# Kernel tuning notes

Hardware: AMD Instinct MI355X
Metric: run time of the kernel (lower is better)

Reference implementation:

```python
import jax, jax.numpy as jnp
import numpy as np
import math

N_HEAD = 32
ROPE_BASE = 10000.0


def _rope_headwise(x):
    # Faithful to the source bug: x is [B, H, S, D] and the rotary module uses
    # x.shape[1] (= H) as the "sequence length", so the angle depends on the
    # head index, broadcast over the true sequence axis.
    B, H, S, D = x.shape
    inv_freq = 1.0 / (ROPE_BASE ** (jnp.arange(0, D, 2, dtype=jnp.float32) / D))  # [D/2]
    t = jnp.arange(H, dtype=jnp.float32)                                          # [H]
    freqs = t[:, None] * inv_freq[None, :]                                        # [H, D/2]
    # emb = cat(freqs, freqs)[..., :D//2] == freqs, so cos/sin are just over freqs
    cos = jnp.cos(freqs)[None, :, None, :]   # [1, H, 1, D/2]
    sin = jnp.sin(freqs)[None, :, None, :]
    x1, x2 = x[..., : D // 2], x[..., D // 2 :]
    return jnp.concatenate([x1 * cos - x2 * sin, x1 * sin + x2 * cos], axis=-1)


def setup_inputs() -> dict:
    key = jax.random.key(0)
    ks = jax.random.split(key, 5)
    B, S, E = 2, 2048, 2048
    scale = 0.02
    return {
        "x": jax.random.normal(ks[0], (B, S, E), dtype=jnp.float32),
        "Wq": jax.random.normal(ks[1], (E, E), dtype=jnp.float32) * scale,
        "bq": jnp.zeros((E,), dtype=jnp.float32),
        "Wk": jax.random.normal(ks[2], (E, E), dtype=jnp.float32) * scale,
        "bk": jnp.zeros((E,), dtype=jnp.float32),
        "Wv": jax.random.normal(ks[3], (E, E), dtype=jnp.float32) * scale,
        "bv": jnp.zeros((E,), dtype=jnp.float32),
        "Wo": jax.random.normal(ks[4], (E, E), dtype=jnp.float32) * scale,
        "bo": jnp.zeros((E,), dtype=jnp.float32),
    }


def reference(x, Wq, bq, Wk, bk, Wv, bv, Wo, bo):
    B, S, E = x.shape
    H = N_HEAD
    D = E // H

    def split_heads(y):  # [B,S,E] -> [B,H,S,D]
        return y.reshape(B, S, H, D).transpose(0, 2, 1, 3)

    q = split_heads(x @ Wq + bq)
    k = split_heads(x @ Wk + bk)
    v = split_heads(x @ Wv + bv)

    q = _rope_headwise(q)
    k = _rope_headwise(k)

    scores = jnp.einsum("bhqd,bhkd->bhqk", q, k) / math.sqrt(D)  # [B,H,S,S]
    causal = jnp.triu(jnp.ones((S, S), dtype=bool), k=1)
    scores = jnp.where(causal[None, None], -jnp.inf, scores)
    attn = jax.nn.softmax(scores, axis=-1)
    out = jnp.einsum("bhqk,bhkd->bhqd", attn, v)                 # [B,H,S,D]
    out = out.transpose(0, 2, 1, 3).reshape(B, S, E)
    return out @ Wo + bo
```

## Files before the change

### kernel.cpp

```cpp
#include <hip/hip_runtime.h>
#include <hip/hip_bf16.h>

#define B_ 2
#define S_ 2048
#define E_ 2048
#define H_ 32
#define M_ (B_*S_)

typedef __bf16 bf16x8 __attribute__((ext_vector_type(8)));
typedef float  f32x4  __attribute__((ext_vector_type(4)));

__device__ __forceinline__ ushort f2bf(float f) {
    uint u = __float_as_uint(f);
    u += 0x7fffu + ((u >> 16) & 1u);
    return (ushort)(u >> 16);
}
__device__ __forceinline__ uint pack2bf(float a, float b) {
    __hip_bfloat162 h = __float22bfloat162_rn(make_float2(a, b));
    return *(uint*)&h;
}
__device__ __forceinline__ float fexp2(float x) {
#if __has_builtin(__builtin_amdgcn_exp2f)
    return __builtin_amdgcn_exp2f(x);
#else
    return exp2f(x);
#endif
}
__device__ __forceinline__ f32x4 f4zero() {
    f32x4 z; z[0]=0.f; z[1]=0.f; z[2]=0.f; z[3]=0.f; return z;
}
__device__ __forceinline__ void async16(const ushort* g, ushort* l) {
    __builtin_amdgcn_global_load_lds((const __attribute__((address_space(1))) void*)g,
                                     (__attribute__((address_space(3))) void*)l, 16, 0, 0);
}

#define NCAST ((M_*E_)/1024)
__global__ __launch_bounds__(256) void prep_kernel(const float* __restrict__ x, ushort* __restrict__ xb,
        const float* __restrict__ W0, const float* __restrict__ W1,
        const float* __restrict__ W2, const float* __restrict__ W3,
        ushort* __restrict__ T0, ushort* __restrict__ T1,
        ushort* __restrict__ T2, ushort* __restrict__ T3) {
    const int bid = blockIdx.x;
    if (bid < NCAST) {
        int i = (bid * 256 + threadIdx.x) * 4;
        float4 v = *(const float4*)(x + i);
        uint2 o;
        o.x = pack2bf(v.x, v.y);
        o.y = pack2bf(v.z, v.w);
        *(uint2*)(xb + i) = o;
        return;
    }
    const int wb = bid - NCAST;
    const int z  = wb >> 10;
    const int rem = wb & 1023;
    const float* W = (z==0)?W0:(z==1)?W1:(z==2)?W2:W3;
    ushort*      T = (z==0)?T0:(z==1)?T1:(z==2)?T2:T3;
    __shared__ float tile[64][65];
    const int k0 = (rem >> 5) * 64, n0 = (rem & 31) * 64;
    const int rr = threadIdx.x >> 4;
    const int cc = (threadIdx.x & 15) * 4;
    #pragma unroll
    for (int p = 0; p < 4; ++p) {
        int r = p * 16 + rr;
        float4 v = *(const float4*)(W + (size_t)(k0 + r) * E_ + n0 + cc);
        tile[r][cc+0] = v.x; tile[r][cc+1] = v.y; tile[r][cc+2] = v.z; tile[r][cc+3] = v.w;
    }
    __syncthreads();
    #pragma unroll
    for (int p = 0; p < 4; ++p) {
        int rn = p * 16 + rr;
        uint2 o;
        o.x = pack2bf(tile[cc+0][rn], tile[cc+1][rn]);
        o.y = pack2bf(tile[cc+2][rn], tile[cc+3][rn]);
        *(uint2*)(T + (size_t)(n0 + rn) * E_ + k0 + cc) = o;
    }
}

#define VMW4 asm volatile("s_waitcnt vmcnt(4)" ::: "memory")
#define VMW0 asm volatile("s_waitcnt vmcnt(0)" ::: "memory")
#define MEMB asm volatile("" ::: "memory")

#define STA_(bf, kt, h) { _Pragma("unroll") for (int it_ = 0; it_ < 2; ++it_) { \
    async16(A + (size_t)(m0 + it_*128 + (h)*64 + srow) * E_ + (kt)*64 + scg*8,  \
            &As[bf][(it_*128 + (h)*64 + wave*8) * 64]); } }

#define STB_(bf, kt, h) { _Pragma("unroll") for (int it_ = 0; it_ < 2; ++it_) { \
    int rih_ = it_*64 + srow;                                                   \
    int ldr_ = ((rih_ >> 5) << 6) + (h)*32 + (rih_ & 31);                       \
    int rwb_ = it_*64 + wave*8;                                                 \
    int wbs_ = ((rwb_ >> 5) << 6) + (h)*32 + (rwb_ & 31);                       \
    async16(Bt + (size_t)(n0 + ldr_) * E_ + (kt)*64 + scg*8,                    \
            &Bs[bf][wbs_ * 64]); } }

#define PH4_(bf, mh, LB, STAGES) {                                              \
    _Pragma("unroll") for (int m_ = 0; m_ < 4; ++m_)                            \
      _Pragma("unroll") for (int k_ = 0; k_ < 2; ++k_) {                        \
        int row_ = wm*128 + (mh)*64 + m_*16 + l15;                              \
        pa[m_][k_] = *(const bf16x8*)(&As[bf][row_*64 + (((k_*4 + quad) ^ (row_ & 7)) << 3)]); } \
    if (LB) {                                                                   \
      _Pragma("unroll") for (int n_ = 0; n_ < 4; ++n_)                          \
        _Pragma("unroll") for (int k_ = 0; k_ < 2; ++k_) {                      \
          int row_ = wn*64 + n_*16 + l15;                                       \
          pb[n_][k_] = *(const bf16x8*)(&Bs[bf][row_*64 + (((k_*4 + quad) ^ (row_ & 7)) << 3)]); } } \
    STAGES;                                                                     \
    MEMB; __builtin_amdgcn_s_barrier();                                         \
    __builtin_amdgcn_s_setprio(1);                                              \
    _Pragma("unroll") for (int k_ = 0; k_ < 2; ++k_)                            \
      _Pragma("unroll") for (int m_ = 0; m_ < 4; ++m_)                          \
        _Pragma("unroll") for (int n_ = 0; n_ < 4; ++n_)                        \
          acc[(mh)*4+m_][n_] = __builtin_amdgcn_mfma_f32_16x16x32_bf16(         \
              pa[m_][k_], pb[n_][k_], acc[(mh)*4+m_][n_], 0, 0, 0);             \
    __builtin_amdgcn_s_setprio(0);                                              \
    asm volatile("s_waitcnt lgkmcnt(0)" ::: "memory");                          \
    __builtin_amdgcn_sched_barrier(0);                                          \
    MEMB; __builtin_amdgcn_s_barrier(); MEMB;                                   \
  }

template<bool OUTF32, bool DOROPE, int NZ>
__global__ __launch_bounds__(512, 2) void gemm256(const ushort* __restrict__ A,
        const ushort* __restrict__ Bt0, const ushort* __restrict__ Bt1, const ushort* __restrict__ Bt2,
        const float* __restrict__ bias0, const float* __restrict__ bias1, const float* __restrict__ bias2,
        void* __restrict__ C0, void* __restrict__ C1, void* __restrict__ C2) {
    const int bid = blockIdx.x;
    const int z   = bid % NZ;
    const int nb  = (bid / NZ) % (E_ / 256);
    const int mb  = bid / (NZ * (E_ / 256));

    const ushort* Bt  = (z==0)?Bt0:(z==1)?Bt1:Bt2;
    const float* bias = (z==0)?bias0:(z==1)?bias1:bias2;
    void* Cv          = (z==0)?C0:(z==1)?C1:C2;

    __shared__ ushort As[2][256 * 64];
    __shared__ ushort Bs[2][256 * 64];

    const int tid  = threadIdx.x;
    const int wave = tid >> 6, lane = tid & 63;
    const int quad = lane >> 4, l15 = lane & 15;
    const int wm = wave >> 2, wn = wave & 3;
    const int m0 = mb * 256, n0 = nb * 256;
    const int srow = tid >> 3;
    const int scg  = (tid & 7) ^ (srow & 7);

    f32x4 acc[8][4];
    #pragma unroll
    for (int i = 0; i < 8; ++i)
        #pragma unroll
        for (int j = 0; j < 4; ++j) acc[i][j] = f4zero();

    bf16x8 pa[4][2];
    bf16x8 pb[4][2];

    STA_(0, 0, 0); STB_(0, 0, 0); STA_(0, 0, 1); STB_(0, 0, 1);
    STA_(1, 1, 0); STB_(1, 1, 0);
    VMW4;
    MEMB; __builtin_amdgcn_s_barrier(); MEMB;

    #pragma unroll 1
    for (int i = 0; i < 15; ++i) {
        const int t1 = 2*i + 1, t2 = 2*i + 2, t3 = 2*i + 3;
        PH4_(0, 0, 1, STB_(1, t1, 1); STA_(1, t1, 1));
        PH4_(0, 1, 0, STA_(0, t2, 0); STB_(0, t2, 0); VMW4);
        PH4_(1, 0, 1, STB_(0, t2, 1); STA_(0, t2, 1));
        PH4_(1, 1, 0, STA_(1, t3, 0); STB_(1, t3, 0); VMW4);
    }
    PH4_(0, 0, 1, STB_(1, 31, 1); STA_(1, 31, 1));
    PH4_(0, 1, 0, VMW0);
    PH4_(1, 0, 1, {});
    PH4_(1, 1, 0, {});

    if (DOROPE && z != 2) {
        const float qsc = (z == 0) ? 0.125f * 1.44269504f : 1.0f;
        const int h = (n0 + wn * 64) >> 6;
        float sn[2], cs[2];
        #pragma unroll
        for (int nt = 0; nt < 2; ++nt) {
            int j = nt * 16 + l15;
            float ang = (float)h * __expf(-(float)j * 0.28782313662425575f);
            __sincosf(ang, &sn[nt], &cs[nt]);
        }
        ushort* C = (ushort*)Cv;
        #pragma unroll
        for (int f = 0; f < 8; ++f) {
            #pragma unroll
            for (int nt = 0; nt < 2; ++nt) {
                int col1 = n0 + wn * 64 + nt * 16 + l15;
                float b1 = bias[col1], b2 = bias[col1 + 32];
                #pragma unroll
                for (int r = 0; r < 4; ++r) {
                    int rowg = m0 + wm * 128 + f * 16 + quad * 4 + r;
                    float x1 = acc[f][nt][r] + b1;
                    float x2 = acc[f][nt + 2][r] + b2;
                    C[(size_t)rowg * E_ + col1]      = f2bf((x1 * cs[nt] - x2 * sn[nt]) * qsc);
                    C[(size_t)rowg * E_ + col1 + 32] = f2bf((x1 * sn[nt] + x2 * cs[nt]) * qsc);
                }
            }
        }
    } else {
        #pragma unroll
        for (int f = 0; f < 8; ++f) {
            #pragma unroll
            for (int nt = 0; nt < 4; ++nt) {
                int col = n0 + wn * 64 + nt * 16 + l15;
                float bv = bias[col];
                #pragma unroll
                for (int r = 0; r < 4; ++r) {
                    int rowg = m0 + wm * 128 + f * 16 + quad * 4 + r;
                    float v = acc[f][nt][r] + bv;
                    if (OUTF32) ((float*)Cv)[(size_t)rowg * E_ + col] = v;
                    else        ((ushort*)Cv)[(size_t)rowg * E_ + col] = f2bf(v);
                }
            }
        }
    }
}
#undef STA_
#undef STB_
#undef PH4_

template<bool OUTF32, bool DOROPE, bool DOVT, int NZ>
__global__ __launch_bounds__(256) void gemm128(const ushort* __restrict__ A,
        const ushort* __restrict__ Bt0, const ushort* __restrict__ Bt1, const ushort* __restrict__ Bt2,
        const float* __restrict__ bias0, const float* __restrict__ bias1, const float* __restrict__ bias2,
        void* __restrict__ C0, void* __restrict__ C1, void* __restrict__ C2) {
    const int bid = blockIdx.x;
    const int z   = bid % NZ;
    const int nb  = (bid / NZ) % (E_ / 128);
    const int mb  = bid / (NZ * (E_ / 128));

    const ushort* Bt  = (z==0)?Bt0:(z==1)?Bt1:Bt2;
    const float* bias = (z==0)?bias0:(z==1)?bias1:bias2;
    void* Cv          = (z==0)?C0:(z==1)?C1:C2;

    __shared__ ushort smem[2 * 128 * 64];
    ushort* As = smem;
    ushort* Bs = smem + 128 * 64;

    const int tid  = threadIdx.x;
    const int wave = tid >> 6, lane = tid & 63;
    const int quad = lane >> 4, l15 = lane & 15;
    const int wm = wave >> 1, wn = wave & 1;
    const int m0 = mb * 128, n0 = nb * 128;
    const int srow = tid >> 3;
    const int scgx = (tid & 7) ^ (srow & 7);

    f32x4 acc[4][4];
    #pragma unroll
    for (int i = 0; i < 4; ++i)
        #pragma unroll
        for (int j = 0; j < 4; ++j) acc[i][j] = f4zero();

    for (int k0 = 0; k0 < E_; k0 += 64) {
        #pragma unroll
        for (int it = 0; it < 4; ++it) {
            int r = it * 32 + srow;
            async16(A  + (size_t)(m0 + r) * E_ + k0 + scgx * 8, As + (it * 256 + wave * 64) * 8);
            async16(Bt + (size_t)(n0 + r) * E_ + k0 + scgx * 8, Bs + (it * 256 + wave * 64) * 8);
        }
        __syncthreads();
        #pragma unroll
        for (int kk = 0; kk < 2; ++kk) {
            bf16x8 af[4], bfr[4];
            #pragma unroll
            for (int mt = 0; mt < 4; ++mt) {
                int row = wm * 64 + mt * 16 + l15;
                af[mt] = *(const bf16x8*)(As + row * 64 + (((kk * 4 + quad) ^ (row & 7)) << 3));
            }
            #pragma unroll
            for (int nt = 0; nt < 4; ++nt) {
                int row = wn * 64 + nt * 16 + l15;
                bfr[nt] = *(const bf16x8*)(Bs + row * 64 + (((kk * 4 + quad) ^ (row & 7)) << 3));
            }
            #pragma unroll
            for (int mt = 0; mt < 4; ++mt)
                #pragma unroll
                for (int nt = 0; nt < 4; ++nt)
                    acc[mt][nt] = __builtin_amdgcn_mfma_f32_16x16x32_bf16(af[mt], bfr[nt], acc[mt][nt], 0, 0, 0);
        }
        __syncthreads();
    }

    if (DOVT) {
        ushort* tbuf = smem;
        ushort* VT = (ushort*)Cv;
        const int b  = m0 >> 11;
        const int s0 = m0 & (S_ - 1);
        #pragma unroll 1
        for (int p = 0; p < 2; ++p) {
            if (wn == p) {
                #pragma unroll
                for (int mt = 0; mt < 4; ++mt)
                    #pragma unroll
                    for (int nt = 0; nt < 4; ++nt) {
                        int cl = nt * 16 + l15;
                        float bv = bias[n0 + p * 64 + cl];
                        #pragma unroll
                        for (int r = 0; r < 4; ++r) {
                            int row = wm * 64 + mt * 16 + quad * 4 + r;
                            tbuf[cl * 136 + row] = f2bf(acc[mt][nt][r] + bv);
                        }
                    }
            }
            __syncthreads();
            {
                int d = tid >> 2, ch = tid & 3;
                int hh = (n0 + p * 64) >> 6;
                const ushort* src = tbuf + d * 136 + ch * 32;
                ushort* dst = VT + ((size_t)(b * H_ + hh) * 64 + d) * S_ + s0 + ch * 32;
                #pragma unroll
                for (int j = 0; j < 4; ++j)
                    *(uint4*)(dst + j * 8) = *(const uint4*)(src + j * 8);
            }
            __syncthreads();
        }
    } else if (DOROPE && z != 2) {
        const float qsc = (z == 0) ? 0.125f * 1.44269504f : 1.0f;
        const int h = (n0 + wn * 64) >> 6;
        float sn[2], cs[2];
        #pragma unroll
        for (int nt = 0; nt < 2; ++nt) {
            int j = nt * 16 + l15;
            float ang = (float)h * __expf(-(float)j * 0.28782313662425575f);
            __sincosf(ang, &sn[nt], &cs[nt]);
        }
        ushort* C = (ushort*)Cv;
        #pragma unroll
        for (int mt = 0; mt < 4; ++mt) {
            #pragma unroll
            for (int nt = 0; nt < 2; ++nt) {
                int col1 = n0 + wn * 64 + nt * 16 + l15;
                float b1 = bias[col1], b2 = bias[col1 + 32];
                #pragma unroll
                for (int r = 0; r < 4; ++r) {
                    int rowg = m0 + wm * 64 + mt * 16 + quad * 4 + r;
                    float x1 = acc[mt][nt][r] + b1;
                    float x2 = acc[mt][nt + 2][r] + b2;
                    C[(size_t)rowg * E_ + col1]      = f2bf((x1 * cs[nt] - x2 * sn[nt]) * qsc);
                    C[(size_t)rowg * E_ + col1 + 32] = f2bf((x1 * sn[nt] + x2 * cs[nt]) * qsc);
                }
            }
        }
    } else {
        #pragma unroll
        for (int mt = 0; mt < 4; ++mt) {
            #pragma unroll
            for (int nt = 0; nt < 4; ++nt) {
                int col = n0 + wn * 64 + nt * 16 + l15;
                float bv = bias[col];
                #pragma unroll
                for (int r = 0; r < 4; ++r) {
                    int rowg = m0 + wm * 64 + mt * 16 + quad * 4 + r;
                    float v = acc[mt][nt][r] + bv;
                    if (OUTF32) ((float*)Cv)[(size_t)rowg * E_ + col] = v;
                    else        ((ushort*)Cv)[(size_t)rowg * E_ + col] = f2bf(v);
                }
            }
        }
    }
}

__global__ __launch_bounds__(512) void flash_kernel(const ushort* __restrict__ qb,
        const ushort* __restrict__ kb, const ushort* __restrict__ vt,
        ushort* __restrict__ ctx) {
    __shared__ ushort KVs[2][2][64 * 64];
    __shared__ ushort Ps[8][16 * 64];

    const int tid  = threadIdx.x;
    const int wave = tid >> 6, lane = tid & 63;
    const int quad = lane >> 4, l15 = lane & 15;
    const int bh = blockIdx.y, b = bh >> 5, h = bh & 31;
    const int srow = tid >> 3;
    const int scgx = (tid & 7) ^ (srow & 7);
    ushort* Pw = Ps[wave];

    bf16x8 ones;
    #pragma unroll
    for (int j = 0; j < 8; ++j) ones[j] = (__bf16)1.0f;

    #pragma unroll 1
    for (int pass = 0; pass < 2; ++pass) {
        const int qx  = pass ? (15 - (int)blockIdx.x) : (int)blockIdx.x;
        const int q0  = qx * 128;
        const int qw0 = q0 + wave * 16;
        const int nkt = 2 * qx + 2;

        bf16x8 qf[2];
        #pragma unroll
        for (int kk = 0; kk < 2; ++kk)
            qf[kk] = *(const bf16x8*)(qb + (size_t)(b * S_ + qw0 + l15) * E_ + h * 64 + kk * 32 + quad * 8);

        f32x4 oacc[4], lacc = f4zero();
        #pragma unroll
        for (int dt = 0; dt < 4; ++dt) oacc[dt] = f4zero();

        async16(kb + (size_t)(b * S_ + srow) * E_ + h * 64 + scgx * 8, KVs[0][0] + wave * 512);
        async16(vt + (size_t)(bh * 64 + srow) * S_ + scgx * 8,         KVs[0][1] + wave * 512);
        __syncthreads();

        #pragma unroll 1
        for (int kt = 0; kt < nkt; ++kt) {
            const int k0 = kt * 64;
            if (kt + 1 < nkt) {
                const int kn = k0 + 64;
                async16(kb + (size_t)(b * S_ + kn + srow) * E_ + h * 64 + scgx * 8,
                        KVs[(kt + 1) & 1][0] + wave * 512);
                async16(vt + (size_t)(bh * 64 + srow) * S_ + kn + scgx * 8,
                        KVs[(kt + 1) & 1][1] + wave * 512);
            }

            if (k0 <= qw0 + 15) {
                const ushort* Ks = KVs[kt & 1][0];
                const ushort* Vs = KVs[kt & 1][1];
                f32x4 sacc[4];
                #pragma unroll
                for (int nt = 0; nt < 4; ++nt) sacc[nt] = f4zero();
                #pragma unroll
                for (int kk = 0; kk < 2; ++kk)
                    #pragma unroll
                    for (int nt = 0; nt < 4; ++nt) {
                        int row = nt * 16 + l15;
                        bf16x8 kf = *(const bf16x8*)(Ks + row * 64 + (((kk * 4 + quad) ^ (row & 7)) << 3));
                        sacc[nt] = __builtin_amdgcn_mfma_f32_16x16x32_bf16(kf, qf[kk], sacc[nt], 0, 0, 0);
                    }

                const bool dm = (k0 + 63 > qw0);
                const int swz = l15 & 7;
                if (dm) {
                    const int q = qw0 + l15;
                    #pragma unroll
                    for (int nt = 0; nt < 4; ++nt) {
                        float p[4];
                        #pragma unroll
                        for (int r = 0; r < 4; ++r) {
                            int s = k0 + nt * 16 + quad * 4 + r;
                            float e = fexp2(sacc[nt][r]);
                            p[r] = (s > q) ? 0.f : e;
                        }
                        uint2 pk;
                        pk.x = pack2bf(p[0], p[1]);
                        pk.y = pack2bf(p[2], p[3]);
                        *(uint2*)(Pw + l15 * 64 + (((nt * 2 + (quad >> 1)) ^ swz) << 3) + (quad & 1) * 4) = pk;
                    }
                } else {
                    #pragma unroll
                    for (int nt = 0; nt < 4; ++nt) {
                        uint2 pk;
                        pk.x = pack2bf(fexp2(sacc[nt][0]), fexp2(sacc[nt][1]));
                        pk.y = pack2bf(fexp2(sacc[nt][2]), fexp2(sacc[nt][3]));
                        *(uint2*)(Pw + l15 * 64 + (((nt * 2 + (quad >> 1)) ^ swz) << 3) + (quad & 1) * 4) = pk;
                    }
                }

                #pragma unroll
                for (int kk = 0; kk < 2; ++kk) {
                    bf16x8 pf = *(const bf16x8*)(Pw + l15 * 64 + (((kk * 4 + quad) ^ swz) << 3));
                    lacc = __builtin_amdgcn_mfma_f32_16x16x32_bf16(pf, ones, lacc, 0, 0, 0);
                    #pragma unroll
                    for (int dt = 0; dt < 4; ++dt) {
                        int row = dt * 16 + l15;
                        bf16x8 vf = *(const bf16x8*)(Vs + row * 64 + (((kk * 4 + quad) ^ (row & 7)) << 3));
                        oacc[dt] = __builtin_amdgcn_mfma_f32_16x16x32_bf16(pf, vf, oacc[dt], 0, 0, 0);
                    }
                }
            }
            __syncthreads();
        }

        #pragma unroll
        for (int r = 0; r < 4; ++r) {
            float inv = 1.0f / lacc[r];
            #pragma unroll
            for (int dt = 0; dt < 4; ++dt)
                ctx[(size_t)(b * S_ + qw0 + quad * 4 + r) * E_ + h * 64 + dt * 16 + l15] =
                    f2bf(oacc[dt][r] * inv);
        }
    }
}

extern "C" void kernel_launch(void* const* d_in, const int* in_sizes, int n_in,
                              void* d_out, int out_size, void* d_ws, size_t ws_size,
                              hipStream_t stream) {
    const float* x  = (const float*)d_in[0];
    const float* Wq = (const float*)d_in[1];
    const float* bq = (const float*)d_in[2];
    const float* Wk = (const float*)d_in[3];
    const float* bk = (const float*)d_in[4];
    const float* Wv = (const float*)d_in[5];
    const float* bv = (const float*)d_in[6];
    const float* Wo = (const float*)d_in[7];
    const float* bo = (const float*)d_in[8];
    float* out = (float*)d_out;

    ushort* p   = (ushort*)d_ws;
    ushort* xb  = p; p += (size_t)M_ * E_;
    ushort* wqt = p; p += (size_t)E_ * E_;
    ushort* wkt = p; p += (size_t)E_ * E_;
    ushort* wvt = p; p += (size_t)E_ * E_;
    ushort* wot = p; p += (size_t)E_ * E_;
    ushort* qb  = p; p += (size_t)M_ * E_;
    ushort* kb  = p; p += (size_t)M_ * E_;
    ushort* vt  = p; p += (size_t)M_ * E_;
    ushort* ctx = p; p += (size_t)M_ * E_;

    prep_kernel<<<NCAST + 4096, 256, 0, stream>>>(x, xb, Wq, Wk, Wv, Wo, wqt, wkt, wvt, wot);
    gemm256<false, true, 2><<<(E_ / 256) * (M_ / 256) * 2, 512, 0, stream>>>(
        xb, wqt, wkt, wkt, bq, bk, bk, qb, kb, kb);
    gemm128<false, false, true, 1><<<(E_ / 128) * (M_ / 128), 256, 0, stream>>>(
        xb, wvt, wvt, wvt, bv, bv, bv, vt, vt, vt);
    flash_kernel<<<dim3(8, B_ * H_), 512, 0, stream>>>(qb, kb, vt, ctx);
    gemm128<true, false, false, 1><<<(E_ / 128) * (M_ / 128), 256, 0, stream>>>(
        ctx, wot, wot, wot, bo, bo, bo, out, out, out);
}
```

Baseline: 359.5 us.

## Rewrite Q/K projection GEMM with 128x256 tiles and register double-buffered LDS reads

Replaces the 256x256-tile Q/K GEMM with a 128x256 tile kernel, which doubles the block count (512 blocks) to fill more CUs. The main loop is restructured so LDS fragment loads for the next k-step go into a second register set while MFMAs consume the current one, with two LDS stages and a deeper vmcnt wait. Each block now reuses less data per tile, so global and LDS traffic per FLOP goes up. Dead RoPE/generic branches are removed from the kernels.

Measured after the change: 369.5 us. +2.8%, slower.

```diff
diff --git a/kernel.cpp b/kernel.cpp
--- a/kernel.cpp
+++ b/kernel.cpp
@@ -76,99 +76,99 @@
     }
 }
 
-#define VMW4 asm volatile("s_waitcnt vmcnt(4)" ::: "memory")
+#define VMW6 asm volatile("s_waitcnt vmcnt(6)" ::: "memory")
 #define VMW0 asm volatile("s_waitcnt vmcnt(0)" ::: "memory")
 #define MEMB asm volatile("" ::: "memory")
 
-#define STA_(bf, kt, h) { _Pragma("unroll") for (int it_ = 0; it_ < 2; ++it_) { \
-    async16(A + (size_t)(m0 + it_*128 + (h)*64 + srow) * E_ + (kt)*64 + scg*8,  \
-            &As[bf][(it_*128 + (h)*64 + wave*8) * 64]); } }
-
-#define STB_(bf, kt, h) { _Pragma("unroll") for (int it_ = 0; it_ < 2; ++it_) { \
-    int rih_ = it_*64 + srow;                                                   \
-    int ldr_ = ((rih_ >> 5) << 6) + (h)*32 + (rih_ & 31);                       \
-    int rwb_ = it_*64 + wave*8;                                                 \
-    int wbs_ = ((rwb_ >> 5) << 6) + (h)*32 + (rwb_ & 31);                       \
-    async16(Bt + (size_t)(n0 + ldr_) * E_ + (kt)*64 + scg*8,                    \
-            &Bs[bf][wbs_ * 64]); } }
-
-#define PH4_(bf, mh, LB, STAGES) {                                              \
+#define QSTA_(bf, kt) { _Pragma("unroll") for (int it_ = 0; it_ < 2; ++it_) {   \
+    async16(A + (size_t)(m0 + it_*64 + srow) * E_ + (kt)*64 + scg*8,            \
+            &As[bf][(it_*64 + wave*8) * 64]); } }
+
+#define QSTB_(bf, kt) { _Pragma("unroll") for (int it_ = 0; it_ < 4; ++it_) {   \
+    async16(Bt + (size_t)(n0 + it_*64 + srow) * E_ + (kt)*64 + scg*8,           \
+            &Bs[bf][(it_*64 + wave*8) * 64]); } }
+
+#define QLOAD_(pa, pb, bf) {                                                    \
     _Pragma("unroll") for (int m_ = 0; m_ < 4; ++m_)                            \
       _Pragma("unroll") for (int k_ = 0; k_ < 2; ++k_) {                        \
-        int row_ = wm*128 + (mh)*64 + m_*16 + l15;                              \
+        int row_ = wm*64 + m_*16 + l15;                                         \
         pa[m_][k_] = *(const bf16x8*)(&As[bf][row_*64 + (((k_*4 + quad) ^ (row_ & 7)) << 3)]); } \
-    if (LB) {                                                                   \
-      _Pragma("unroll") for (int n_ = 0; n_ < 4; ++n_)                          \
-        _Pragma("unroll") for (int k_ = 0; k_ < 2; ++k_) {                      \
-          int row_ = wn*64 + n_*16 + l15;                                       \
-          pb[n_][k_] = *(const bf16x8*)(&Bs[bf][row_*64 + (((k_*4 + quad) ^ (row_ & 7)) << 3)]); } } \
-    STAGES;                                                                     \
-    MEMB; __builtin_amdgcn_s_barrier();                                         \
+    _Pragma("unroll") for (int n_ = 0; n_ < 4; ++n_)                            \
+      _Pragma("unroll") for (int k_ = 0; k_ < 2; ++k_) {                        \
+        int row_ = wn*64 + n_*16 + l15;                                         \
+        pb[n_][k_] = *(const bf16x8*)(&Bs[bf][row_*64 + (((k_*4 + quad) ^ (row_ & 7)) << 3)]); } }
+
+#define QMM_(pa, pb) {                                                          \
     __builtin_amdgcn_s_setprio(1);                                              \
     _Pragma("unroll") for (int k_ = 0; k_ < 2; ++k_)                            \
       _Pragma("unroll") for (int m_ = 0; m_ < 4; ++m_)                          \
         _Pragma("unroll") for (int n_ = 0; n_ < 4; ++n_)                        \
-          acc[(mh)*4+m_][n_] = __builtin_amdgcn_mfma_f32_16x16x32_bf16(         \
-              pa[m_][k_], pb[n_][k_], acc[(mh)*4+m_][n_], 0, 0, 0);             \
+          acc[m_][n_] = __builtin_amdgcn_mfma_f32_16x16x32_bf16(                \
+              pa[m_][k_], pb[n_][k_], acc[m_][n_], 0, 0, 0);                    \
     __builtin_amdgcn_s_setprio(0);                                              \
+  }
+
+#define QPH_(STG, VM, ca, cb, na, nb_, DORD, rdbf) {                            \
+    STG; VM;                                                                    \
+    MEMB; __builtin_amdgcn_s_barrier();                                         \
+    if (DORD) QLOAD_(na, nb_, rdbf);                                            \
+    QMM_(ca, cb);                                                               \
     asm volatile("s_waitcnt lgkmcnt(0)" ::: "memory");                          \
     __builtin_amdgcn_sched_barrier(0);                                          \
     MEMB; __builtin_amdgcn_s_barrier(); MEMB;                                   \
   }
 
-template<bool OUTF32, bool DOROPE, int NZ>
-__global__ __launch_bounds__(512, 2) void gemm256(const ushort* __restrict__ A,
-        const ushort* __restrict__ Bt0, const ushort* __restrict__ Bt1, const ushort* __restrict__ Bt2,
-        const float* __restrict__ bias0, const float* __restrict__ bias1, const float* __restrict__ bias2,
-        void* __restrict__ C0, void* __restrict__ C1, void* __restrict__ C2) {
+template<int NZ>
+__global__ __launch_bounds__(512, 2) void gemm_qk(const ushort* __restrict__ A,
+        const ushort* __restrict__ Bt0, const ushort* __restrict__ Bt1,
+        const float* __restrict__ bias0, const float* __restrict__ bias1,
+        void* __restrict__ C0, void* __restrict__ C1) {
     const int bid = blockIdx.x;
     const int z   = bid % NZ;
     const int nb  = (bid / NZ) % (E_ / 256);
     const int mb  = bid / (NZ * (E_ / 256));
 
-    const ushort* Bt  = (z==0)?Bt0:(z==1)?Bt1:Bt2;
-    const float* bias = (z==0)?bias0:(z==1)?bias1:bias2;
-    void* Cv          = (z==0)?C0:(z==1)?C1:C2;
-
-    __shared__ ushort As[2][256 * 64];
+    const ushort* Bt  = (z==0)?Bt0:Bt1;
+    const float* bias = (z==0)?bias0:bias1;
+    void* Cv          = (z==0)?C0:C1;
+
+    __shared__ ushort As[2][128 * 64];
     __shared__ ushort Bs[2][256 * 64];
 
     const int tid  = threadIdx.x;
     const int wave = tid >> 6, lane = tid & 63;
     const int quad = lane >> 4, l15 = lane & 15;
     const int wm = wave >> 2, wn = wave & 3;
-    const int m0 = mb * 256, n0 = nb * 256;
+    const int m0 = mb * 128, n0 = nb * 256;
     const int srow = tid >> 3;
     const int scg  = (tid & 7) ^ (srow & 7);
 
-    f32x4 acc[8][4];
+    f32x4 acc[4][4];
     #pragma unroll
-    for (int i = 0; i < 8; ++i)
+    for (int i = 0; i < 4; ++i)
         #pragma unroll
         for (int j = 0; j < 4; ++j) acc[i][j] = f4zero();
 
-    bf16x8 pa[4][2];
-    bf16x8 pb[4][2];
-
-    STA_(0, 0, 0); STB_(0, 0, 0); STA_(0, 0, 1); STB_(0, 0, 1);
-    STA_(1, 1, 0); STB_(1, 1, 0);
-    VMW4;
+    bf16x8 a0[4][2], b0[4][2], a1[4][2], b1[4][2];
+
+    QSTA_(0, 0); QSTB_(0, 0);
+    QSTA_(1, 1); QSTB_(1, 1);
+    VMW6;
+    MEMB; __builtin_amdgcn_s_barrier(); MEMB;
+    QLOAD_(a0, b0, 0);
+    asm volatile("s_waitcnt lgkmcnt(0)" ::: "memory");
+    __builtin_amdgcn_sched_barrier(0);
     MEMB; __builtin_amdgcn_s_barrier(); MEMB;
 
     #pragma unroll 1
     for (int i = 0; i < 15; ++i) {
-        const int t1 = 2*i + 1, t2 = 2*i + 2, t3 = 2*i + 3;
-        PH4_(0, 0, 1, STB_(1, t1, 1); STA_(1, t1, 1));
-        PH4_(0, 1, 0, STA_(0, t2, 0); STB_(0, t2, 0); VMW4);
-        PH4_(1, 0, 1, STB_(0, t2, 1); STA_(0, t2, 1));
-        PH4_(1, 1, 0, STA_(1, t3, 0); STB_(1, t3, 0); VMW4);
-    }
-    PH4_(0, 0, 1, STB_(1, 31, 1); STA_(1, 31, 1));
-    PH4_(0, 1, 0, VMW0);
-    PH4_(1, 0, 1, {});
-    PH4_(1, 1, 0, {});
-
-    if (DOROPE && z != 2) {
+        QPH_(QSTA_(0, 2*i + 2); QSTB_(0, 2*i + 2), VMW6, a0, b0, a1, b1, 1, 1);
+        QPH_(QSTA_(1, 2*i + 3); QSTB_(1, 2*i + 3), VMW6, a1, b1, a0, b0, 1, 0);
+    }
+    QPH_({}, VMW0, a0, b0, a1, b1, 1, 1);
+    QPH_({}, {}, a1, b1, a0, b0, 0, 0);
+
+    {
         const float qsc = (z == 0) ? 0.125f * 1.44269504f : 1.0f;
         const int h = (n0 + wn * 64) >> 6;
         float sn[2], cs[2];
@@ -180,44 +180,30 @@
         }
         ushort* C = (ushort*)Cv;
         #pragma unroll
-        for (int f = 0; f < 8; ++f) {
+        for (int m = 0; m < 4; ++m) {
             #pragma unroll
             for (int nt = 0; nt < 2; ++nt) {
                 int col1 = n0 + wn * 64 + nt * 16 + l15;
-                float b1 = bias[col1], b2 = bias[col1 + 32];
+                float b1v = bias[col1], b2v = bias[col1 + 32];
                 #pragma unroll
                 for (int r = 0; r < 4; ++r) {
-                    int rowg = m0 + wm * 128 + f * 16 + quad * 4 + r;
-                    float x1 = acc[f][nt][r] + b1;
-                    float x2 = acc[f][nt + 2][r] + b2;
+                    int rowg = m0 + wm * 64 + m * 16 + quad * 4 + r;
+                    float x1 = acc[m][nt][r] + b1v;
+                    float x2 = acc[m][nt + 2][r] + b2v;
                     C[(size_t)rowg * E_ + col1]      = f2bf((x1 * cs[nt] - x2 * sn[nt]) * qsc);
                     C[(size_t)rowg * E_ + col1 + 32] = f2bf((x1 * sn[nt] + x2 * cs[nt]) * qsc);
                 }
             }
         }
-    } else {
-        #pragma unroll
-        for (int f = 0; f < 8; ++f) {
-            #pragma unroll
-            for (int nt = 0; nt < 4; ++nt) {
-                int col = n0 + wn * 64 + nt * 16 + l15;
-                float bv = bias[col];
-                #pragma unroll
-                for (int r = 0; r < 4; ++r) {
-                    int rowg = m0 + wm * 128 + f * 16 + quad * 4 + r;
-                    float v = acc[f][nt][r] + bv;
-                    if (OUTF32) ((float*)Cv)[(size_t)rowg * E_ + col] = v;
-                    else        ((ushort*)Cv)[(size_t)rowg * E_ + col] = f2bf(v);
-                }
-            }
-        }
-    }
-}
-#undef STA_
-#undef STB_
-#undef PH4_
-
-template<bool OUTF32, bool DOROPE, bool DOVT, int NZ>
+    }
+}
+#undef QSTA_
+#undef QSTB_
+#undef QLOAD_
+#undef QMM_
+#undef QPH_
+
+template<bool OUTF32, bool DOVT, int NZ>
 __global__ __launch_bounds__(256) void gemm128(const ushort* __restrict__ A,
         const ushort* __restrict__ Bt0, const ushort* __restrict__ Bt1, const ushort* __restrict__ Bt2,
         const float* __restrict__ bias0, const float* __restrict__ bias1, const float* __restrict__ bias2,
@@ -311,33 +297,6 @@
                     *(uint4*)(dst + j * 8) = *(const uint4*)(src + j * 8);
             }
             __syncthreads();
-        }
-    } else if (DOROPE && z != 2) {
-        const float qsc = (z == 0) ? 0.125f * 1.44269504f : 1.0f;
-        const int h = (n0 + wn * 64) >> 6;
-        float sn[2], cs[2];
-        #pragma unroll
-        for (int nt = 0; nt < 2; ++nt) {
-            int j = nt * 16 + l15;
-            float ang = (float)h * __expf(-(float)j * 0.28782313662425575f);
-            __sincosf(ang, &sn[nt], &cs[nt]);
-        }
-        ushort* C = (ushort*)Cv;
-        #pragma unroll
-        for (int mt = 0; mt < 4; ++mt) {
-            #pragma unroll
-            for (int nt = 0; nt < 2; ++nt) {
-                int col1 = n0 + wn * 64 + nt * 16 + l15;
-                float b1 = bias[col1], b2 = bias[col1 + 32];
-                #pragma unroll
-                for (int r = 0; r < 4; ++r) {
-                    int rowg = m0 + wm * 64 + mt * 16 + quad * 4 + r;
-                    float x1 = acc[mt][nt][r] + b1;
-                    float x2 = acc[mt][nt + 2][r] + b2;
-                    C[(size_t)rowg * E_ + col1]      = f2bf((x1 * cs[nt] - x2 * sn[nt]) * qsc);
-                    C[(size_t)rowg * E_ + col1 + 32] = f2bf((x1 * sn[nt] + x2 * cs[nt]) * qsc);
-                }
-            }
         }
     } else {
         #pragma unroll
@@ -502,11 +461,11 @@
     ushort* ctx = p; p += (size_t)M_ * E_;
 
     prep_kernel<<<NCAST + 4096, 256, 0, stream>>>(x, xb, Wq, Wk, Wv, Wo, wqt, wkt, wvt, wot);
-    gemm256<false, true, 2><<<(E_ / 256) * (M_ / 256) * 2, 512, 0, stream>>>(
-        xb, wqt, wkt, wkt, bq, bk, bk, qb, kb, kb);
-    gemm128<false, false, true, 1><<<(E_ / 128) * (M_ / 128), 256, 0, stream>>>(
+    gemm_qk<2><<<(M_ / 128) * (E_ / 256) * 2, 512, 0, stream>>>(
+        xb, wqt, wkt, bq, bk, qb, kb);
+    gemm128<false, true, 1><<<(E_ / 128) * (M_ / 128), 256, 0, stream>>>(
         xb, wvt, wvt, wvt, bv, bv, bv, vt, vt, vt);
     flash_kernel<<<dim3(8, B_ * H_), 512, 0, stream>>>(qb, kb, vt, ctx);
-    gemm128<true, false, false, 1><<<(E_ / 128) * (M_ / 128), 256, 0, stream>>>(
+    gemm128<true, false, 1><<<(E_ / 128) * (M_ / 128), 256, 0, stream>>>(
         ctx, wot, wot, wot, bo, bo, bo, out, out, out);
 }
```
